# Performance work log

Hardware: AMD Instinct MI355X
Metric: run time of the kernel (lower is better)

Reference implementation:

```python
import jax, jax.numpy as jnp
import numpy as np

D_MODEL = 1024
D_INNER = 2048        # expand=2
D_STATE = 128
NHEADS = 16           # d_inner / headdim
HEADDIM = 128
D_CONV = 4
D_XBC = D_INNER + 2 * D_STATE          # 2304 (ngroups=1)
D_IN_PROJ = 2 * D_INNER + 2 * D_STATE + NHEADS  # 4368
BATCH, SEQLEN = 2, 2048
EPS = 1e-5


def setup_inputs() -> dict:
    key = jax.random.key(0)
    ks = jax.random.split(key, 8)
    f = jnp.float32
    return {
        "x": jax.random.normal(ks[0], (BATCH, SEQLEN, D_MODEL), f),
        "ln_w": jnp.ones((D_MODEL,), f),
        "ln_b": jnp.zeros((D_MODEL,), f),
        "W_in": jax.random.normal(ks[1], (D_MODEL, D_IN_PROJ), f) * 0.02,
        "conv_w": jax.random.normal(ks[2], (D_XBC, D_CONV), f) * 0.2,
        "conv_b": jnp.zeros((D_XBC,), f),
        "dt_bias": jax.random.uniform(ks[3], (NHEADS,), f, -4.0, -2.0),
        "A_log": jnp.log(jax.random.uniform(ks[4], (NHEADS,), f, 1.0, 16.0)),
        "D": jnp.ones((NHEADS,), f),
        "rms_w": jnp.ones((D_INNER,), f),
        "W_out": jax.random.normal(ks[5], (D_INNER, D_MODEL), f) * 0.02,
    }


def _mamba_wrap(x, ln_w, ln_b, W_in, conv_w, conv_b, dt_bias, A_log, D, rms_w, W_out):
    B, L = x.shape[0], x.shape[1]
    # LayerNorm (pre-norm)
    mu = jnp.mean(x, -1, keepdims=True)
    var = jnp.mean(jnp.square(x - mu), -1, keepdims=True)
    xn = (x - mu) * jax.lax.rsqrt(var + EPS) * ln_w + ln_b
    # input projection -> z, xBC, dt
    zxbcdt = xn @ W_in                               # (B,L,4368)
    z = zxbcdt[..., :D_INNER]                        # (B,L,2048)
    xBC = zxbcdt[..., D_INNER:D_INNER + D_XBC]       # (B,L,2304)
    dt = jax.nn.softplus(zxbcdt[..., -NHEADS:] + dt_bias)  # (B,L,16)
    # causal depthwise conv1d (kernel 4), then SiLU
    xp = jnp.pad(xBC, ((0, 0), (D_CONV - 1, 0), (0, 0)))
    taps = jnp.stack([xp[:, k:k + L, :] for k in range(D_CONV)], axis=-1)  # (B,L,C,K)
    xBC = jax.nn.silu(jnp.einsum('blck,ck->blc', taps, conv_w) + conv_b)
    # split into SSM inputs
    xh = xBC[..., :D_INNER].reshape(B, L, NHEADS, HEADDIM)   # (B,L,H,P)
    Bm = xBC[..., D_INNER:D_INNER + D_STATE]                  # (B,L,N) ngroups=1
    Cm = xBC[..., D_INNER + D_STATE:]                         # (B,L,N)
    A = -jnp.exp(A_log)                                       # (H,)
    dA = jnp.exp(dt * A)                                      # (B,L,H)

    def step(state, inp):
        xt, dtt, dAt, Bt, Ct = inp  # (B,H,P),(B,H),(B,H),(B,N),(B,N)
        state = state * dAt[..., None, None] + (dtt[..., None] * xt)[..., None] * Bt[:, None, None, :]
        y = jnp.einsum('bhpn,bn->bhp', state, Ct)
        return state, y

    init = jnp.zeros((B, NHEADS, HEADDIM, D_STATE), x.dtype)
    xs = (xh.transpose(1, 0, 2, 3), dt.transpose(1, 0, 2), dA.transpose(1, 0, 2),
          Bm.transpose(1, 0, 2), Cm.transpose(1, 0, 2))
    _, ys = jax.lax.scan(step, init, xs)                      # (L,B,H,P)
    y = ys.transpose(1, 0, 2, 3) + D[None, None, :, None] * xh  # skip term
    y = y.reshape(B, L, D_INNER)
    # gated RMSNorm: rmsnorm(y * silu(z)) * weight
    y = y * jax.nn.silu(z)
    y = y * jax.lax.rsqrt(jnp.mean(y * y, -1, keepdims=True) + EPS) * rms_w
    # output projection + residual
    return x + y @ W_out


def reference(x, ln_w, ln_b, W_in, conv_w, conv_b, dt_bias, A_log, D, rms_w, W_out):
    return _mamba_wrap(x, ln_w, ln_b, W_in, conv_w, conv_b, dt_bias, A_log, D, rms_w, W_out)
```

## Files before the change

kernel.cpp:

```cpp
#include <hip/hip_runtime.h>

typedef unsigned short ushort_t;
typedef __attribute__((ext_vector_type(8))) unsigned short ushort8;
typedef __attribute__((ext_vector_type(4))) unsigned short ushortv4;
typedef __attribute__((ext_vector_type(8))) __bf16 bf16x8;
typedef __attribute__((ext_vector_type(4))) float f32x4;

#define BATCH   2
#define SEQLEN  2048
#define BL      4096
#define DMODEL  1024
#define DINNER  2048
#define DSTATE  128
#define NHEADS  16
#define DXBC    2304
#define DPROJ   4368
#define NPAD    4480
#define EPSF    1e-5f
#define QCH     128
#define NCH     16
#define BH      32

#define SWZ(row, colbyte) ((colbyte) ^ (((row) & 7) << 4))

#define GLDS(gp, lp) __builtin_amdgcn_global_load_lds( \
    (const __attribute__((address_space(1))) void*)(gp), \
    (__attribute__((address_space(3))) void*)(lp), 16, 0, 0)

__device__ __forceinline__ float bf2f(ushort_t h) {
    unsigned int u = ((unsigned int)h) << 16;
    float f; __builtin_memcpy(&f, &u, 4); return f;
}
__device__ __forceinline__ ushort_t f2bf(float f) {
    unsigned int u; __builtin_memcpy(&u, &f, 4);
    unsigned int r = u + 0x7fffu + ((u >> 16) & 1u);
    return (ushort_t)(r >> 16);
}
__device__ __forceinline__ float siluf(float x) { return x / (1.f + expf(-x)); }
__device__ __forceinline__ float softplusf(float x) { return (x > 20.f) ? x : log1pf(expf(x)); }

__global__ __launch_bounds__(256) void ln_kernel(const float* __restrict__ x,
        const float* __restrict__ w, const float* __restrict__ b, ushort_t* __restrict__ xn) {
    int r = blockIdx.x, t = threadIdx.x;
    const float* xr = x + (size_t)r * DMODEL;
    float4 v = *(const float4*)&xr[t * 4];
    float s  = v.x + v.y + v.z + v.w;
    float sq = v.x*v.x + v.y*v.y + v.z*v.z + v.w*v.w;
    __shared__ float red[8];
    #pragma unroll
    for (int m = 32; m >= 1; m >>= 1) { s += __shfl_xor(s, m, 64); sq += __shfl_xor(sq, m, 64); }
    int wv = t >> 6;
    if ((t & 63) == 0) { red[wv] = s; red[4 + wv] = sq; }
    __syncthreads();
    s  = red[0] + red[1] + red[2] + red[3];
    sq = red[4] + red[5] + red[6] + red[7];
    float mu  = s * (1.f / DMODEL);
    float var = sq * (1.f / DMODEL) - mu * mu;
    float inv = rsqrtf(var + EPSF);
    float4 wv4 = *(const float4*)&w[t * 4];
    float4 bv4 = *(const float4*)&b[t * 4];
    ushortv4 o;
    o[0] = f2bf((v.x - mu) * inv * wv4.x + bv4.x);
    o[1] = f2bf((v.y - mu) * inv * wv4.y + bv4.y);
    o[2] = f2bf((v.z - mu) * inv * wv4.z + bv4.z);
    o[3] = f2bf((v.w - mu) * inv * wv4.w + bv4.w);
    *(ushortv4*)&xn[(size_t)r * DMODEL + t * 4] = o;
}

__global__ __launch_bounds__(256) void transpose_cast(const float* __restrict__ W,
        ushort_t* __restrict__ WT, int K, int N) {
    __shared__ float tile[32][33];
    int n0 = blockIdx.x * 32, k0 = blockIdx.y * 32;
    int tx = threadIdx.x & 31, ty = threadIdx.x >> 5;
    #pragma unroll
    for (int i = 0; i < 32; i += 8) {
        int n = n0 + tx;
        tile[ty + i][tx] = (n < N) ? W[(size_t)(k0 + ty + i) * N + n] : 0.f;
    }
    __syncthreads();
    #pragma unroll
    for (int i = 0; i < 32; i += 8) {
        WT[(size_t)(n0 + ty + i) * K + k0 + tx] = f2bf(tile[tx][ty + i]);
    }
}

__global__ __launch_bounds__(256) void gemm_bt(const ushort_t* __restrict__ A,
        const ushort_t* __restrict__ BT, float* __restrict__ C,
        const float* __restrict__ resid, int K, int ldc, int nbx) {
    const int tid = threadIdx.x;
    const int nwg = gridDim.x;
    const int cpx = nwg >> 3;
    const int lid = (blockIdx.x & 7) * cpx + (blockIdx.x >> 3);
    const int m0 = (lid / nbx) * 128, n0 = (lid % nbx) * 128;
    __shared__ ushort_t As[2][128 * 32];
    __shared__ ushort_t Bs[2][128 * 32];
    const int lane = tid & 63, wave = tid >> 6;
    const int wrow = wave * 32;
    const int srow = lane >> 2;
    const int selm = (lane & 3) * 8;
    const ushort_t* ag0 = A  + (size_t)(m0 + wrow + srow) * K + selm;
    const ushort_t* ag1 = ag0 + (size_t)16 * K;
    const ushort_t* bg0 = BT + (size_t)(n0 + wrow + srow) * K + selm;
    const ushort_t* bg1 = bg0 + (size_t)16 * K;
    const int wm = (wave >> 1) * 64, wn = (wave & 1) * 64;
    const int fr = lane & 15, ko = (lane >> 4) * 8;
    f32x4 acc[4][4];
    #pragma unroll
    for (int i = 0; i < 4; i++)
        #pragma unroll
        for (int j = 0; j < 4; j++) acc[i][j] = (f32x4){0.f, 0.f, 0.f, 0.f};
    GLDS(ag0, &As[0][wrow * 32]);
    GLDS(ag1, &As[0][(wrow + 16) * 32]);
    GLDS(bg0, &Bs[0][wrow * 32]);
    GLDS(bg1, &Bs[0][(wrow + 16) * 32]);
    __syncthreads();
    int cur = 0;
    for (int k0 = 0; k0 < K; k0 += 32) {
        const int nxt = cur ^ 1;
        if (k0 + 32 < K) {
            GLDS(ag0 + k0 + 32, &As[nxt][wrow * 32]);
            GLDS(ag1 + k0 + 32, &As[nxt][(wrow + 16) * 32]);
            GLDS(bg0 + k0 + 32, &Bs[nxt][wrow * 32]);
            GLDS(bg1 + k0 + 32, &Bs[nxt][(wrow + 16) * 32]);
        }
        bf16x8 af[4], bfr[4];
        #pragma unroll
        for (int i = 0; i < 4; i++) af[i]  = *(const bf16x8*)&As[cur][(wm + i * 16 + fr) * 32 + ko];
        #pragma unroll
        for (int j = 0; j < 4; j++) bfr[j] = *(const bf16x8*)&Bs[cur][(wn + j * 16 + fr) * 32 + ko];
        #pragma unroll
        for (int i = 0; i < 4; i++)
            #pragma unroll
            for (int j = 0; j < 4; j++)
                acc[i][j] = __builtin_amdgcn_mfma_f32_16x16x32_bf16(af[i], bfr[j], acc[i][j], 0, 0, 0);
        __syncthreads();
        cur = nxt;
    }
    const int r0 = (lane >> 4) * 4;
    #pragma unroll
    for (int i = 0; i < 4; i++)
        #pragma unroll
        for (int j = 0; j < 4; j++)
            #pragma unroll
            for (int r = 0; r < 4; r++) {
                int m = m0 + wm + i * 16 + r0 + r;
                int n = n0 + wn + j * 16 + fr;
                float v = acc[i][j][r];
                if (resid) v += resid[(size_t)m * ldc + n];
                C[(size_t)m * ldc + n] = v;
            }
}

__global__ __launch_bounds__(256) void conv_kernel(const float* __restrict__ zxb,
        const float* __restrict__ conv_w, const float* __restrict__ conv_b,
        const float* __restrict__ dt_bias, const float* __restrict__ A_log,
        ushort_t* __restrict__ xcv, ushort_t* __restrict__ Bcg, ushort_t* __restrict__ Ccg,
        float* __restrict__ dtv, float* __restrict__ dta) {
    int bid = blockIdx.x;
    int l = bid & (SEQLEN - 1);
    int tid = threadIdx.x;
    const float* rowp = zxb + (size_t)bid * NPAD;
    #pragma unroll 1
    for (int i = 0; i < 9; i++) {
        int c = tid + i * 256;
        float acc = conv_b[c];
        #pragma unroll
        for (int k = 0; k < 4; k++) {
            int ll = l - 3 + k;
            if (ll >= 0) acc += rowp[(ptrdiff_t)(k - 3) * NPAD + DINNER + c] * conv_w[c * 4 + k];
        }
        float v = siluf(acc);
        if (c < DINNER)                xcv[(size_t)bid * DINNER + c] = f2bf(v);
        else if (c < DINNER + DSTATE)  Bcg[(size_t)bid * DSTATE + (c - DINNER)] = f2bf(v);
        else                           Ccg[(size_t)bid * DSTATE + (c - DINNER - DSTATE)] = f2bf(v);
    }
    if (tid < NHEADS) {
        float raw = rowp[DINNER + DXBC + tid] + dt_bias[tid];
        float dt = softplusf(raw);
        float A = -expf(A_log[tid]);
        dtv[(size_t)bid * NHEADS + tid] = dt;
        dta[(size_t)bid * NHEADS + tid] = dt * A;
    }
}

__global__ __launch_bounds__(128) void cumsum_kernel(const float* __restrict__ dta,
        const float* __restrict__ dtv, float* __restrict__ cabuf, float* __restrict__ expca,
        float* __restrict__ wbuf, float* __restrict__ dtbuf, float* __restrict__ dtot) {
    const int c = blockIdx.x, h = blockIdx.y, b = blockIdx.z;
    const int bh = b * NHEADS + h;
    const int j = threadIdx.x;
    const size_t row = (size_t)b * SEQLEN + c * QCH + j;
    float v  = dta[row * NHEADS + h];
    float dt = dtv[row * NHEADS + h];
    float pv = v;
    #pragma unroll
    for (int off = 1; off < 64; off <<= 1) {
        float u = __shfl_up(pv, off, 64);
        if ((j & 63) >= off) pv += u;
    }
    __shared__ float wsum[2];
    if ((j & 63) == 63) wsum[j >> 6] = pv;
    __syncthreads();
    float tot = wsum[0] + wsum[1];
    if (j >= 64) pv += wsum[0];
    const size_t idx = ((size_t)bh * NCH + c) * QCH + j;
    cabuf[idx] = pv;
    expca[idx] = expf(pv);
    wbuf[idx]  = expf(tot - pv) * dt;
    dtbuf[idx] = dt;
    if (j == 0) dtot[bh * NCH + c] = expf(tot);
}

__global__ __launch_bounds__(256) void chunkstate_kernel(const ushort_t* __restrict__ xcv,
        const ushort_t* __restrict__ Bcg, const float* __restrict__ wbuf,
        float* __restrict__ states) {
    const int c = blockIdx.x, h = blockIdx.y, b = blockIdx.z;
    const int bh = b * NHEADS + h;
    const int tid = threadIdx.x;
    __shared__ ushort_t Xt[128 * 128];
    __shared__ ushort_t Bt[128 * 128];
    __shared__ float wsh[QCH];
    if (tid < QCH) wsh[tid] = wbuf[((size_t)bh * NCH + c) * QCH + tid];
    __syncthreads();
    const size_t row0 = (size_t)b * SEQLEN + c * QCH;
    {
        const int f = tid & 127;
        const int jh = (tid >> 7) * 64;
        const ushort_t* xsrc = xcv + (row0 + jh) * DINNER + h * 128 + f;
        const ushort_t* bsrc = Bcg + (row0 + jh) * DSTATE + f;
        char* xrow = (char*)Xt + f * 256;
        char* brow = (char*)Bt + f * 256;
        #pragma unroll 2
        for (int e8 = 0; e8 < 8; e8++) {
            ushort8 tx, tb;
            #pragma unroll
            for (int e = 0; e < 8; e++) {
                int j = e8 * 8 + e;
                tx[e] = xsrc[(size_t)j * DINNER];
                tb[e] = f2bf(bf2f(bsrc[(size_t)j * DSTATE]) * wsh[jh + j]);
            }
            int cb = (jh + e8 * 8) * 2;
            *(ushort8*)(xrow + SWZ(f, cb)) = tx;
            *(ushort8*)(brow + SWZ(f, cb)) = tb;
        }
    }
    __syncthreads();
    const int lane = tid & 63, wave = tid >> 6;
    const int wp = (wave >> 1) * 64, wn = (wave & 1) * 64;
    const int fr = lane & 15, ko = (lane >> 4) * 8;
    f32x4 acc[4][4];
    #pragma unroll
    for (int i = 0; i < 4; i++)
        #pragma unroll
        for (int j = 0; j < 4; j++) acc[i][j] = (f32x4){0.f, 0.f, 0.f, 0.f};
    for (int k0 = 0; k0 < 128; k0 += 32) {
        bf16x8 af[4], bfr[4];
        #pragma unroll
        for (int i = 0; i < 4; i++) {
            int rp = wp + i * 16 + fr;
            af[i] = *(const bf16x8*)((const char*)Xt + rp * 256 + SWZ(rp, (k0 + ko) * 2));
        }
        #pragma unroll
        for (int j = 0; j < 4; j++) {
            int rn = wn + j * 16 + fr;
            bfr[j] = *(const bf16x8*)((const char*)Bt + rn * 256 + SWZ(rn, (k0 + ko) * 2));
        }
        #pragma unroll
        for (int i = 0; i < 4; i++)
            #pragma unroll
            for (int j = 0; j < 4; j++)
                acc[i][j] = __builtin_amdgcn_mfma_f32_16x16x32_bf16(af[i], bfr[j], acc[i][j], 0, 0, 0);
    }
    const int r0 = (lane >> 4) * 4;
    float* outp = states + ((size_t)bh * NCH + c) * 16384;
    #pragma unroll
    for (int i = 0; i < 4; i++)
        #pragma unroll
        for (int j = 0; j < 4; j++)
            #pragma unroll
            for (int r = 0; r < 4; r++)
                outp[(wp + i * 16 + r0 + r) * 128 + wn + j * 16 + fr] = acc[i][j][r];
}

__global__ __launch_bounds__(256) void statescan_kernel(float* __restrict__ states,
        const float* __restrict__ dtot) {
    const int pseg = blockIdx.x, bh = blockIdx.y;
    const int tid = threadIdx.x;
    const int p = pseg * 8 + (tid >> 5);
    const int n4 = (tid & 31) * 4;
    float* base = states + (size_t)bh * NCH * 16384 + p * 128 + n4;
    const float* dtp = dtot + bh * NCH;
    f32x4 run = (f32x4){0.f, 0.f, 0.f, 0.f};
    #pragma unroll 1
    for (int c = 0; c < NCH; c++) {
        f32x4* ptr = (f32x4*)(base + (size_t)c * 16384);
        f32x4 cs = *ptr;
        *ptr = run;
        float d = dtp[c];
        run = run * d + cs;
    }
}

__global__ __launch_bounds__(256) void chunkout_kernel(const ushort_t* __restrict__ xcv,
        const ushort_t* __restrict__ Bcg, const ushort_t* __restrict__ Ccg,
        const float* __restrict__ states, const float* __restrict__ cabuf,
        const float* __restrict__ expca, const float* __restrict__ dtbuf,
        const float* __restrict__ Dvec, ushort_t* __restrict__ yv) {
    const int c = blockIdx.x, h = blockIdx.y, b = blockIdx.z;
    const int bh = b * NHEADS + h;
    const int tid = threadIdx.x;
    __shared__ ushort_t R1[128 * 128];
    __shared__ ushort_t R2[128 * 128];
    __shared__ ushort_t R3[128 * 128];
    __shared__ float cash[QCH], dtsh[QCH], exsh[QCH];
    const size_t aidx = ((size_t)bh * NCH + c) * QCH;
    if (tid < QCH) {
        cash[tid] = cabuf[aidx + tid];
        dtsh[tid] = dtbuf[aidx + tid];
        exsh[tid] = expca[aidx + tid];
    }
    const size_t row0 = (size_t)b * SEQLEN + c * QCH;
    #pragma unroll
    for (int it = 0; it < 8; it++) {
        int g = tid + it * 256;
        int r = g >> 4, n8 = (g & 15) * 8;
        ushort8 vb = *(const ushort8*)&Bcg[(row0 + r) * DSTATE + n8];
        ushort8 vc = *(const ushort8*)&Ccg[(row0 + r) * DSTATE + n8];
        int cb = n8 * 2;
        *(ushort8*)((char*)R1 + r * 256 + SWZ(r, cb)) = vb;
        *(ushort8*)((char*)R2 + r * 256 + SWZ(r, cb)) = vc;
    }
    __syncthreads();
    const int lane = tid & 63, wave = tid >> 6;
    const int fr = lane & 15, ko = (lane >> 4) * 8, r0 = (lane >> 4) * 4;
    const int wj = (wave >> 1) * 64, wt = (wave & 1) * 64;
    f32x4 g_[4][4];
    #pragma unroll
    for (int i = 0; i < 4; i++)
        #pragma unroll
        for (int t = 0; t < 4; t++) g_[i][t] = (f32x4){0.f, 0.f, 0.f, 0.f};
    if (!(wj == 64 && wt == 0)) {
        for (int k0 = 0; k0 < 128; k0 += 32) {
            bf16x8 af[4], bfr[4];
            #pragma unroll
            for (int i = 0; i < 4; i++) {
                int rj = wj + i * 16 + fr;
                af[i] = *(const bf16x8*)((const char*)R1 + rj * 256 + SWZ(rj, (k0 + ko) * 2));
            }
            #pragma unroll
            for (int t = 0; t < 4; t++) {
                int rt = wt + t * 16 + fr;
                bfr[t] = *(const bf16x8*)((const char*)R2 + rt * 256 + SWZ(rt, (k0 + ko) * 2));
            }
            #pragma unroll
            for (int i = 0; i < 4; i++)
                #pragma unroll
                for (int t = 0; t < 4; t++)
                    g_[i][t] = __builtin_amdgcn_mfma_f32_16x16x32_bf16(af[i], bfr[t], g_[i][t], 0, 0, 0);
        }
    }
    const float Dh = Dvec[h];
    #pragma unroll
    for (int i = 0; i < 4; i++) {
        #pragma unroll
        for (int t = 0; t < 4; t++) {
            int tt = wt + t * 16 + fr;
            int jj0 = wj + i * 16 + r0;
            ushortv4 pk;
            #pragma unroll
            for (int r = 0; r < 4; r++) {
                int jj = jj0 + r;
                float val = 0.f;
                if (jj <= tt) {
                    val = g_[i][t][r] * expf(cash[tt] - cash[jj]) * dtsh[jj];
                    if (jj == tt) val += Dh;
                }
                pk[r] = f2bf(val);
            }
            *(ushortv4*)((char*)R3 + tt * 256 + SWZ(tt, jj0 * 2)) = pk;
        }
    }
    __syncthreads();
    {
        const float* sp = states + ((size_t)bh * NCH + c) * 16384;
        #pragma unroll
        for (int it = 0; it < 8; it++) {
            int g = tid + it * 256;
            int p = g >> 4, n8 = (g & 15) * 8;
            f32x4 a = *(const f32x4*)&sp[p * 128 + n8];
            f32x4 bq = *(const f32x4*)&sp[p * 128 + n8 + 4];
            ushort8 v;
            v[0] = f2bf(a[0]);  v[1] = f2bf(a[1]);  v[2] = f2bf(a[2]);  v[3] = f2bf(a[3]);
            v[4] = f2bf(bq[0]); v[5] = f2bf(bq[1]); v[6] = f2bf(bq[2]); v[7] = f2bf(bq[3]);
            *(ushort8*)((char*)R1 + p * 256 + SWZ(p, n8 * 2)) = v;
        }
    }
    __syncthreads();
    const int wty = (wave >> 1) * 64, wpy = (wave & 1) * 64;
    f32x4 y_[4][4];
    #pragma unroll
    for (int i = 0; i < 4; i++)
        #pragma unroll
        for (int j = 0; j < 4; j++) y_[i][j] = (f32x4){0.f, 0.f, 0.f, 0.f};
    for (int k0 = 0; k0 < 128; k0 += 32) {
        bf16x8 af[4], bfr[4];
        #pragma unroll
        for (int i = 0; i < 4; i++) {
            int rt = wty + i * 16 + fr;
            af[i] = *(const bf16x8*)((const char*)R2 + rt * 256 + SWZ(rt, (k0 + ko) * 2));
        }
        #pragma unroll
        for (int j = 0; j < 4; j++) {
            int rp = wpy + j * 16 + fr;
            bfr[j] = *(const bf16x8*)((const char*)R1 + rp * 256 + SWZ(rp, (k0 + ko) * 2));
        }
        #pragma unroll
        for (int i = 0; i < 4; i++)
            #pragma unroll
            for (int j = 0; j < 4; j++)
                y_[i][j] = __builtin_amdgcn_mfma_f32_16x16x32_bf16(af[i], bfr[j], y_[i][j], 0, 0, 0);
    }
    #pragma unroll
    for (int i = 0; i < 4; i++)
        #pragma unroll
        for (int r = 0; r < 4; r++) {
            float sc = exsh[wty + i * 16 + r0 + r];
            #pragma unroll
            for (int j = 0; j < 4; j++) y_[i][j][r] *= sc;
        }
    __syncthreads();
    {
        const int f = tid & 127;
        const int jh = (tid >> 7) * 64;
        const ushort_t* xsrc = xcv + (row0 + jh) * DINNER + h * 128 + f;
        char* xrow = (char*)R1 + f * 256;
        #pragma unroll 2
        for (int e8 = 0; e8 < 8; e8++) {
            ushort8 tx;
            #pragma unroll
            for (int e = 0; e < 8; e++) tx[e] = xsrc[(size_t)(e8 * 8 + e) * DINNER];
            int cb = (jh + e8 * 8) * 2;
            *(ushort8*)(xrow + SWZ(f, cb)) = tx;
        }
    }
    __syncthreads();
    const int kmax = wty + 64;
    for (int k0 = 0; k0 < kmax; k0 += 32) {
        bf16x8 af[4], bfr[4];
        #pragma unroll
        for (int i = 0; i < 4; i++) {
            int rt = wty + i * 16 + fr;
            af[i] = *(const bf16x8*)((const char*)R3 + rt * 256 + SWZ(rt, (k0 + ko) * 2));
        }
        #pragma unroll
        for (int j = 0; j < 4; j++) {
            int rp = wpy + j * 16 + fr;
            bfr[j] = *(const bf16x8*)((const char*)R1 + rp * 256 + SWZ(rp, (k0 + ko) * 2));
        }
        #pragma unroll
        for (int i = 0; i < 4; i++)
            #pragma unroll
            for (int j = 0; j < 4; j++)
                y_[i][j] = __builtin_amdgcn_mfma_f32_16x16x32_bf16(af[i], bfr[j], y_[i][j], 0, 0, 0);
    }
    #pragma unroll
    for (int i = 0; i < 4; i++)
        #pragma unroll
        for (int j = 0; j < 4; j++)
            #pragma unroll
            for (int r = 0; r < 4; r++) {
                int t = wty + i * 16 + r0 + r;
                int p = wpy + j * 16 + fr;
                yv[(row0 + t) * DINNER + h * 128 + p] = f2bf(y_[i][j][r]);
            }
}

__global__ __launch_bounds__(256) void gate_rms(const ushort_t* __restrict__ yv,
        const float* __restrict__ zxb, const float* __restrict__ rms_w,
        ushort_t* __restrict__ ynorm) {
    int r = blockIdx.x, t = threadIdx.x;
    const ushort_t* yr = yv + (size_t)r * DINNER;
    const float* zr = zxb + (size_t)r * NPAD;
    ushort8 y8 = *(const ushort8*)&yr[t * 8];
    float4 z0 = *(const float4*)&zr[t * 8];
    float4 z1 = *(const float4*)&zr[t * 8 + 4];
    float g[8];
    g[0] = bf2f((ushort_t)y8[0]) * siluf(z0.x);
    g[1] = bf2f((ushort_t)y8[1]) * siluf(z0.y);
    g[2] = bf2f((ushort_t)y8[2]) * siluf(z0.z);
    g[3] = bf2f((ushort_t)y8[3]) * siluf(z0.w);
    g[4] = bf2f((ushort_t)y8[4]) * siluf(z1.x);
    g[5] = bf2f((ushort_t)y8[5]) * siluf(z1.y);
    g[6] = bf2f((ushort_t)y8[6]) * siluf(z1.z);
    g[7] = bf2f((ushort_t)y8[7]) * siluf(z1.w);
    float sq = 0.f;
    #pragma unroll
    for (int j = 0; j < 8; j++) sq += g[j] * g[j];
    __shared__ float red[4];
    #pragma unroll
    for (int m = 32; m >= 1; m >>= 1) sq += __shfl_xor(sq, m, 64);
    int wv = t >> 6;
    if ((t & 63) == 0) red[wv] = sq;
    __syncthreads();
    sq = red[0] + red[1] + red[2] + red[3];
    float scale = rsqrtf(sq * (1.f / DINNER) + EPSF);
    float4 w0 = *(const float4*)&rms_w[t * 8];
    float4 w1 = *(const float4*)&rms_w[t * 8 + 4];
    ushort8 o;
    o[0] = f2bf(g[0] * scale * w0.x);
    o[1] = f2bf(g[1] * scale * w0.y);
    o[2] = f2bf(g[2] * scale * w0.z);
    o[3] = f2bf(g[3] * scale * w0.w);
    o[4] = f2bf(g[4] * scale * w1.x);
    o[5] = f2bf(g[5] * scale * w1.y);
    o[6] = f2bf(g[6] * scale * w1.z);
    o[7] = f2bf(g[7] * scale * w1.w);
    *(ushort8*)&ynorm[(size_t)r * DINNER + t * 8] = o;
}

extern "C" void kernel_launch(void* const* d_in, const int* in_sizes, int n_in,
                              void* d_out, int out_size, void* d_ws, size_t ws_size,
                              hipStream_t stream) {
    (void)in_sizes; (void)n_in; (void)out_size; (void)ws_size;
    const float* x       = (const float*)d_in[0];
    const float* ln_w    = (const float*)d_in[1];
    const float* ln_b    = (const float*)d_in[2];
    const float* W_in    = (const float*)d_in[3];
    const float* conv_w  = (const float*)d_in[4];
    const float* conv_b  = (const float*)d_in[5];
    const float* dt_bias = (const float*)d_in[6];
    const float* A_log   = (const float*)d_in[7];
    const float* Dvec    = (const float*)d_in[8];
    const float* rms_w   = (const float*)d_in[9];
    const float* W_out   = (const float*)d_in[10];
    float* out = (float*)d_out;

    char* ws = (char*)d_ws;
    size_t off = 0;
    auto alloc = [&](size_t bytes) -> void* {
        void* p = ws + off;
        off += (bytes + 255) & ~(size_t)255;
        return p;
    };
    ushort_t* xn    = (ushort_t*)alloc((size_t)BL * DMODEL * 2);
    ushort_t* WinT  = (ushort_t*)alloc((size_t)NPAD * DMODEL * 2);
    float*    zxb   = (float*)   alloc((size_t)BL * NPAD * 4);
    ushort_t* xcv   = (ushort_t*)alloc((size_t)BL * DINNER * 2);
    ushort_t* Bcg   = (ushort_t*)alloc((size_t)BL * DSTATE * 2);
    ushort_t* Ccg   = (ushort_t*)alloc((size_t)BL * DSTATE * 2);
    float*    dtv   = (float*)   alloc((size_t)BL * NHEADS * 4);
    float*    dta   = (float*)   alloc((size_t)BL * NHEADS * 4);
    ushort_t* yv    = (ushort_t*)alloc((size_t)BL * DINNER * 2);
    ushort_t* ynorm = (ushort_t*)alloc((size_t)BL * DINNER * 2);
    ushort_t* WoutT = (ushort_t*)alloc((size_t)DMODEL * DINNER * 2);
    float*    cabuf = (float*)   alloc((size_t)BH * NCH * QCH * 4);
    float*    expcb = (float*)   alloc((size_t)BH * NCH * QCH * 4);
    float*    wbuf  = (float*)   alloc((size_t)BH * NCH * QCH * 4);
    float*    dtbuf = (float*)   alloc((size_t)BH * NCH * QCH * 4);
    float*    dtot  = (float*)   alloc((size_t)BH * NCH * 4);
    float*    states= (float*)   alloc((size_t)BH * NCH * 16384 * 4);

    ln_kernel<<<BL, 256, 0, stream>>>(x, ln_w, ln_b, xn);
    transpose_cast<<<dim3(NPAD / 32, DMODEL / 32), 256, 0, stream>>>(W_in, WinT, DMODEL, DPROJ);
    transpose_cast<<<dim3(DMODEL / 32, DINNER / 32), 256, 0, stream>>>(W_out, WoutT, DINNER, DMODEL);
    gemm_bt<<<(NPAD / 128) * (BL / 128), 256, 0, stream>>>(xn, WinT, zxb, nullptr, DMODEL, NPAD, NPAD / 128);
    conv_kernel<<<BL, 256, 0, stream>>>(zxb, conv_w, conv_b, dt_bias, A_log, xcv, Bcg, Ccg, dtv, dta);
    cumsum_kernel<<<dim3(NCH, NHEADS, BATCH), 128, 0, stream>>>(dta, dtv, cabuf, expcb, wbuf, dtbuf, dtot);
    chunkstate_kernel<<<dim3(NCH, NHEADS, BATCH), 256, 0, stream>>>(xcv, Bcg, wbuf, states);
    statescan_kernel<<<dim3(16, BH), 256, 0, stream>>>(states, dtot);
    chunkout_kernel<<<dim3(NCH, NHEADS, BATCH), 256, 0, stream>>>(xcv, Bcg, Ccg, states, cabuf, expcb, dtbuf, Dvec, yv);
    gate_rms<<<BL, 256, 0, stream>>>(yv, zxb, rms_w, ynorm);
    gemm_bt<<<(DMODEL / 128) * (BL / 128), 256, 0, stream>>>(ynorm, WoutT, out, x, DINNER, DMODEL, DMODEL / 128);
}
```

Measured before the change: 247.7 us.

## Deepen GEMM LDS pipeline to four stages with explicit vmcnt waits

The bf16 GEMM's shared-memory staging moves from double-buffering to a four-buffer ring that keeps three k-tiles of global-to-LDS loads in flight. Each iteration waits only on the oldest tile's loads through a partial s_waitcnt vmcnt before a raw s_barrier, instead of a full __syncthreads. This is meant to hide global-load latency behind the MFMA work. LDS use doubles to 64KB per block, which can lower occupancy. Correctness depends on the GLDS macro issuing exactly four vm ops per stage so that the vmcnt thresholds match.

Measured after the change: 261.7 us. 5.6% more time.

```diff
diff --git a/kernel.cpp b/kernel.cpp
--- a/kernel.cpp
+++ b/kernel.cpp
@@ -84,6 +84,15 @@
     }
 }
 
+#define STAGE_T(t) do { \
+    const int _b = (t) & 3; \
+    const size_t _ko = (size_t)(t) * 32; \
+    GLDS(ag0 + _ko, &As[_b][wrow * 32]); \
+    GLDS(ag1 + _ko, &As[_b][(wrow + 16) * 32]); \
+    GLDS(bg0 + _ko, &Bs[_b][wrow * 32]); \
+    GLDS(bg1 + _ko, &Bs[_b][(wrow + 16) * 32]); \
+} while (0)
+
 __global__ __launch_bounds__(256) void gemm_bt(const ushort_t* __restrict__ A,
         const ushort_t* __restrict__ BT, float* __restrict__ C,
         const float* __restrict__ resid, int K, int ldc, int nbx) {
@@ -92,8 +101,8 @@
     const int cpx = nwg >> 3;
     const int lid = (blockIdx.x & 7) * cpx + (blockIdx.x >> 3);
     const int m0 = (lid / nbx) * 128, n0 = (lid % nbx) * 128;
-    __shared__ ushort_t As[2][128 * 32];
-    __shared__ ushort_t Bs[2][128 * 32];
+    __shared__ ushort_t As[4][128 * 32];
+    __shared__ ushort_t Bs[4][128 * 32];
     const int lane = tid & 63, wave = tid >> 6;
     const int wrow = wave * 32;
     const int srow = lane >> 2;
@@ -109,32 +118,27 @@
     for (int i = 0; i < 4; i++)
         #pragma unroll
         for (int j = 0; j < 4; j++) acc[i][j] = (f32x4){0.f, 0.f, 0.f, 0.f};
-    GLDS(ag0, &As[0][wrow * 32]);
-    GLDS(ag1, &As[0][(wrow + 16) * 32]);
-    GLDS(bg0, &Bs[0][wrow * 32]);
-    GLDS(bg1, &Bs[0][(wrow + 16) * 32]);
-    __syncthreads();
-    int cur = 0;
-    for (int k0 = 0; k0 < K; k0 += 32) {
-        const int nxt = cur ^ 1;
-        if (k0 + 32 < K) {
-            GLDS(ag0 + k0 + 32, &As[nxt][wrow * 32]);
-            GLDS(ag1 + k0 + 32, &As[nxt][(wrow + 16) * 32]);
-            GLDS(bg0 + k0 + 32, &Bs[nxt][wrow * 32]);
-            GLDS(bg1 + k0 + 32, &Bs[nxt][(wrow + 16) * 32]);
-        }
+    const int nt = K >> 5;
+    STAGE_T(0); STAGE_T(1); STAGE_T(2);
+    asm volatile("s_waitcnt vmcnt(8)" ::: "memory");
+    __builtin_amdgcn_s_barrier();
+    for (int t = 0; t < nt; ++t) {
+        const int b = t & 3;
+        if (t + 3 < nt) STAGE_T(t + 3);
         bf16x8 af[4], bfr[4];
         #pragma unroll
-        for (int i = 0; i < 4; i++) af[i]  = *(const bf16x8*)&As[cur][(wm + i * 16 + fr) * 32 + ko];
-        #pragma unroll
-        for (int j = 0; j < 4; j++) bfr[j] = *(const bf16x8*)&Bs[cur][(wn + j * 16 + fr) * 32 + ko];
+        for (int i = 0; i < 4; i++) af[i]  = *(const bf16x8*)&As[b][(wm + i * 16 + fr) * 32 + ko];
+        #pragma unroll
+        for (int j = 0; j < 4; j++) bfr[j] = *(const bf16x8*)&Bs[b][(wn + j * 16 + fr) * 32 + ko];
         #pragma unroll
         for (int i = 0; i < 4; i++)
             #pragma unroll
             for (int j = 0; j < 4; j++)
                 acc[i][j] = __builtin_amdgcn_mfma_f32_16x16x32_bf16(af[i], bfr[j], acc[i][j], 0, 0, 0);
-        __syncthreads();
-        cur = nxt;
+        if (t + 3 < nt)      asm volatile("s_waitcnt vmcnt(8)" ::: "memory");
+        else if (t + 2 < nt) asm volatile("s_waitcnt vmcnt(4)" ::: "memory");
+        else if (t + 1 < nt) asm volatile("s_waitcnt vmcnt(0)" ::: "memory");
+        __builtin_amdgcn_s_barrier();
     }
     const int r0 = (lane >> 4) * 4;
     #pragma unroll
```

## Store in-proj output and chunk states in bf16 to halve intermediate traffic

Applied to the files above, without the earlier changes.

The input-projection GEMM now writes its 4096x4480 output as bf16 instead of fp32, and the conv and gate kernels read bf16, with the conv kernel also vectorised to 8 channels per thread. Per-chunk SSM states are stored as bf16 too, and the state scan carries its running sum in fp32 registers while reading and writing bf16. This roughly halves the bytes moved through the largest intermediates. The cost is reduced precision on z, xBC, dt and the chunk states, which may affect accuracy, especially for the pre-softplus dt value and the accumulated states.

After: 267.5 us. 1.08x slower.

```diff
diff --git a/kernel.cpp b/kernel.cpp
--- a/kernel.cpp
+++ b/kernel.cpp
@@ -84,8 +84,9 @@
     }
 }
 
+template <bool OUTBF>
 __global__ __launch_bounds__(256) void gemm_bt(const ushort_t* __restrict__ A,
-        const ushort_t* __restrict__ BT, float* __restrict__ C,
+        const ushort_t* __restrict__ BT, void* __restrict__ Cv,
         const float* __restrict__ resid, int K, int ldc, int nbx) {
     const int tid = threadIdx.x;
     const int nwg = gridDim.x;
@@ -146,12 +147,16 @@
                 int m = m0 + wm + i * 16 + r0 + r;
                 int n = n0 + wn + j * 16 + fr;
                 float v = acc[i][j][r];
-                if (resid) v += resid[(size_t)m * ldc + n];
-                C[(size_t)m * ldc + n] = v;
-            }
-}
-
-__global__ __launch_bounds__(256) void conv_kernel(const float* __restrict__ zxb,
+                if (OUTBF) {
+                    ((ushort_t*)Cv)[(size_t)m * ldc + n] = f2bf(v);
+                } else {
+                    if (resid) v += resid[(size_t)m * ldc + n];
+                    ((float*)Cv)[(size_t)m * ldc + n] = v;
+                }
+            }
+}
+
+__global__ __launch_bounds__(256) void conv_kernel(const ushort_t* __restrict__ zxb,
         const float* __restrict__ conv_w, const float* __restrict__ conv_b,
         const float* __restrict__ dt_bias, const float* __restrict__ A_log,
         ushort_t* __restrict__ xcv, ushort_t* __restrict__ Bcg, ushort_t* __restrict__ Ccg,
@@ -159,23 +164,36 @@
     int bid = blockIdx.x;
     int l = bid & (SEQLEN - 1);
     int tid = threadIdx.x;
-    const float* rowp = zxb + (size_t)bid * NPAD;
+    const ushort_t* rowp = zxb + (size_t)bid * NPAD;
     #pragma unroll 1
-    for (int i = 0; i < 9; i++) {
-        int c = tid + i * 256;
-        float acc = conv_b[c];
+    for (int u = tid; u < DXBC / 8; u += 256) {
+        int c0 = u * 8;
+        float acc[8];
+        {
+            float4 b0 = *(const float4*)&conv_b[c0];
+            float4 b1 = *(const float4*)&conv_b[c0 + 4];
+            acc[0] = b0.x; acc[1] = b0.y; acc[2] = b0.z; acc[3] = b0.w;
+            acc[4] = b1.x; acc[5] = b1.y; acc[6] = b1.z; acc[7] = b1.w;
+        }
         #pragma unroll
         for (int k = 0; k < 4; k++) {
             int ll = l - 3 + k;
-            if (ll >= 0) acc += rowp[(ptrdiff_t)(k - 3) * NPAD + DINNER + c] * conv_w[c * 4 + k];
-        }
-        float v = siluf(acc);
-        if (c < DINNER)                xcv[(size_t)bid * DINNER + c] = f2bf(v);
-        else if (c < DINNER + DSTATE)  Bcg[(size_t)bid * DSTATE + (c - DINNER)] = f2bf(v);
-        else                           Ccg[(size_t)bid * DSTATE + (c - DINNER - DSTATE)] = f2bf(v);
+            if (ll >= 0) {
+                ushort8 xv = *(const ushort8*)&rowp[(ptrdiff_t)(k - 3) * NPAD + DINNER + c0];
+                #pragma unroll
+                for (int e = 0; e < 8; e++)
+                    acc[e] += bf2f((ushort_t)xv[e]) * conv_w[(c0 + e) * 4 + k];
+            }
+        }
+        ushort8 o;
+        #pragma unroll
+        for (int e = 0; e < 8; e++) o[e] = f2bf(siluf(acc[e]));
+        if (c0 < DINNER)                *(ushort8*)&xcv[(size_t)bid * DINNER + c0] = o;
+        else if (c0 < DINNER + DSTATE)  *(ushort8*)&Bcg[(size_t)bid * DSTATE + (c0 - DINNER)] = o;
+        else                            *(ushort8*)&Ccg[(size_t)bid * DSTATE + (c0 - DINNER - DSTATE)] = o;
     }
     if (tid < NHEADS) {
-        float raw = rowp[DINNER + DXBC + tid] + dt_bias[tid];
+        float raw = bf2f(rowp[DINNER + DXBC + tid]) + dt_bias[tid];
         float dt = softplusf(raw);
         float A = -expf(A_log[tid]);
         dtv[(size_t)bid * NHEADS + tid] = dt;
@@ -213,7 +231,7 @@
 
 __global__ __launch_bounds__(256) void chunkstate_kernel(const ushort_t* __restrict__ xcv,
         const ushort_t* __restrict__ Bcg, const float* __restrict__ wbuf,
-        float* __restrict__ states) {
+        ushort_t* __restrict__ states) {
     const int c = blockIdx.x, h = blockIdx.y, b = blockIdx.z;
     const int bh = b * NHEADS + h;
     const int tid = threadIdx.x;
@@ -272,38 +290,43 @@
                 acc[i][j] = __builtin_amdgcn_mfma_f32_16x16x32_bf16(af[i], bfr[j], acc[i][j], 0, 0, 0);
     }
     const int r0 = (lane >> 4) * 4;
-    float* outp = states + ((size_t)bh * NCH + c) * 16384;
+    ushort_t* outp = states + ((size_t)bh * NCH + c) * 16384;
     #pragma unroll
     for (int i = 0; i < 4; i++)
         #pragma unroll
         for (int j = 0; j < 4; j++)
             #pragma unroll
             for (int r = 0; r < 4; r++)
-                outp[(wp + i * 16 + r0 + r) * 128 + wn + j * 16 + fr] = acc[i][j][r];
-}
-
-__global__ __launch_bounds__(256) void statescan_kernel(float* __restrict__ states,
+                outp[(wp + i * 16 + r0 + r) * 128 + wn + j * 16 + fr] = f2bf(acc[i][j][r]);
+}
+
+__global__ __launch_bounds__(256) void statescan_kernel(ushort_t* __restrict__ states,
         const float* __restrict__ dtot) {
     const int pseg = blockIdx.x, bh = blockIdx.y;
     const int tid = threadIdx.x;
     const int p = pseg * 8 + (tid >> 5);
     const int n4 = (tid & 31) * 4;
-    float* base = states + (size_t)bh * NCH * 16384 + p * 128 + n4;
+    ushort_t* base = states + (size_t)bh * NCH * 16384 + p * 128 + n4;
     const float* dtp = dtot + bh * NCH;
-    f32x4 run = (f32x4){0.f, 0.f, 0.f, 0.f};
+    float r0 = 0.f, r1 = 0.f, r2 = 0.f, r3 = 0.f;
     #pragma unroll 1
     for (int c = 0; c < NCH; c++) {
-        f32x4* ptr = (f32x4*)(base + (size_t)c * 16384);
-        f32x4 cs = *ptr;
-        *ptr = run;
+        ushortv4* ptr = (ushortv4*)(base + (size_t)c * 16384);
+        ushortv4 cs = *ptr;
+        ushortv4 o;
+        o[0] = f2bf(r0); o[1] = f2bf(r1); o[2] = f2bf(r2); o[3] = f2bf(r3);
+        *ptr = o;
         float d = dtp[c];
-        run = run * d + cs;
+        r0 = r0 * d + bf2f(cs[0]);
+        r1 = r1 * d + bf2f(cs[1]);
+        r2 = r2 * d + bf2f(cs[2]);
+        r3 = r3 * d + bf2f(cs[3]);
     }
 }
 
 __global__ __launch_bounds__(256) void chunkout_kernel(const ushort_t* __restrict__ xcv,
         const ushort_t* __restrict__ Bcg, const ushort_t* __restrict__ Ccg,
-        const float* __restrict__ states, const float* __restrict__ cabuf,
+        const ushort_t* __restrict__ states, const float* __restrict__ cabuf,
         const float* __restrict__ expca, const float* __restrict__ dtbuf,
         const float* __restrict__ Dvec, ushort_t* __restrict__ yv) {
     const int c = blockIdx.x, h = blockIdx.y, b = blockIdx.z;
@@ -382,16 +405,12 @@
     }
     __syncthreads();
     {
-        const float* sp = states + ((size_t)bh * NCH + c) * 16384;
+        const ushort_t* sp = states + ((size_t)bh * NCH + c) * 16384;
         #pragma unroll
         for (int it = 0; it < 8; it++) {
             int g = tid + it * 256;
             int p = g >> 4, n8 = (g & 15) * 8;
-            f32x4 a = *(const f32x4*)&sp[p * 128 + n8];
-            f32x4 bq = *(const f32x4*)&sp[p * 128 + n8 + 4];
-            ushort8 v;
-            v[0] = f2bf(a[0]);  v[1] = f2bf(a[1]);  v[2] = f2bf(a[2]);  v[3] = f2bf(a[3]);
-            v[4] = f2bf(bq[0]); v[5] = f2bf(bq[1]); v[6] = f2bf(bq[2]); v[7] = f2bf(bq[3]);
+            ushort8 v = *(const ushort8*)&sp[p * 128 + n8];
             *(ushort8*)((char*)R1 + p * 256 + SWZ(p, n8 * 2)) = v;
         }
     }
@@ -476,23 +495,17 @@
 }
 
 __global__ __launch_bounds__(256) void gate_rms(const ushort_t* __restrict__ yv,
-        const float* __restrict__ zxb, const float* __restrict__ rms_w,
+        const ushort_t* __restrict__ zxb, const float* __restrict__ rms_w,
         ushort_t* __restrict__ ynorm) {
     int r = blockIdx.x, t = threadIdx.x;
     const ushort_t* yr = yv + (size_t)r * DINNER;
-    const float* zr = zxb + (size_t)r * NPAD;
+    const ushort_t* zr = zxb + (size_t)r * NPAD;
     ushort8 y8 = *(const ushort8*)&yr[t * 8];
-    float4 z0 = *(const float4*)&zr[t * 8];
-    float4 z1 = *(const float4*)&zr[t * 8 + 4];
+    ushort8 z8 = *(const ushort8*)&zr[t * 8];
     float g[8];
-    g[0] = bf2f((ushort_t)y8[0]) * siluf(z0.x);
-    g[1] = bf2f((ushort_t)y8[1]) * siluf(z0.y);
-    g[2] = bf2f((ushort_t)y8[2]) * siluf(z0.z);
-    g[3] = bf2f((ushort_t)y8[3]) * siluf(z0.w);
-    g[4] = bf2f((ushort_t)y8[4]) * siluf(z1.x);
-    g[5] = bf2f((ushort_t)y8[5]) * siluf(z1.y);
-    g[6] = bf2f((ushort_t)y8[6]) * siluf(z1.z);
-    g[7] = bf2f((ushort_t)y8[7]) * siluf(z1.w);
+    #pragma unroll
+    for (int j = 0; j < 8; j++)
+        g[j] = bf2f((ushort_t)y8[j]) * siluf(bf2f((ushort_t)z8[j]));
     float sq = 0.f;
     #pragma unroll
     for (int j = 0; j < 8; j++) sq += g[j] * g[j];
@@ -544,7 +557,7 @@
     };
     ushort_t* xn    = (ushort_t*)alloc((size_t)BL * DMODEL * 2);
     ushort_t* WinT  = (ushort_t*)alloc((size_t)NPAD * DMODEL * 2);
-    float*    zxb   = (float*)   alloc((size_t)BL * NPAD * 4);
+    ushort_t* zxb   = (ushort_t*)alloc((size_t)BL * NPAD * 2);
     ushort_t* xcv   = (ushort_t*)alloc((size_t)BL * DINNER * 2);
     ushort_t* Bcg   = (ushort_t*)alloc((size_t)BL * DSTATE * 2);
     ushort_t* Ccg   = (ushort_t*)alloc((size_t)BL * DSTATE * 2);
@@ -558,17 +571,17 @@
     float*    wbuf  = (float*)   alloc((size_t)BH * NCH * QCH * 4);
     float*    dtbuf = (float*)   alloc((size_t)BH * NCH * QCH * 4);
     float*    dtot  = (float*)   alloc((size_t)BH * NCH * 4);
-    float*    states= (float*)   alloc((size_t)BH * NCH * 16384 * 4);
+    ushort_t* states= (ushort_t*)alloc((size_t)BH * NCH * 16384 * 2);
 
     ln_kernel<<<BL, 256, 0, stream>>>(x, ln_w, ln_b, xn);
     transpose_cast<<<dim3(NPAD / 32, DMODEL / 32), 256, 0, stream>>>(W_in, WinT, DMODEL, DPROJ);
     transpose_cast<<<dim3(DMODEL / 32, DINNER / 32), 256, 0, stream>>>(W_out, WoutT, DINNER, DMODEL);
-    gemm_bt<<<(NPAD / 128) * (BL / 128), 256, 0, stream>>>(xn, WinT, zxb, nullptr, DMODEL, NPAD, NPAD / 128);
+    gemm_bt<true><<<(NPAD / 128) * (BL / 128), 256, 0, stream>>>(xn, WinT, zxb, nullptr, DMODEL, NPAD, NPAD / 128);
     conv_kernel<<<BL, 256, 0, stream>>>(zxb, conv_w, conv_b, dt_bias, A_log, xcv, Bcg, Ccg, dtv, dta);
     cumsum_kernel<<<dim3(NCH, NHEADS, BATCH), 128, 0, stream>>>(dta, dtv, cabuf, expcb, wbuf, dtbuf, dtot);
     chunkstate_kernel<<<dim3(NCH, NHEADS, BATCH), 256, 0, stream>>>(xcv, Bcg, wbuf, states);
     statescan_kernel<<<dim3(16, BH), 256, 0, stream>>>(states, dtot);
     chunkout_kernel<<<dim3(NCH, NHEADS, BATCH), 256, 0, stream>>>(xcv, Bcg, Ccg, states, cabuf, expcb, dtbuf, Dvec, yv);
     gate_rms<<<BL, 256, 0, stream>>>(yv, zxb, rms_w, ynorm);
-    gemm_bt<<<(DMODEL / 128) * (BL / 128), 256, 0, stream>>>(ynorm, WoutT, out, x, DINNER, DMODEL, DMODEL / 128);
-}
+    gemm_bt<false><<<(DMODEL / 128) * (BL / 128), 256, 0, stream>>>(ynorm, WoutT, out, x, DINNER, DMODEL, DMODEL / 128);
+}
```
